# Kernel optimization log

Measured on AMD Instinct MI355X. Metric: run time of the kernel, lower is better.

The kernel has to match this reference:

```python
import jax, jax.numpy as jnp
import numpy as np

NEG_SLOPE_MLP = 0.1   # F.leaky_relu(x, 0.1) used throughout the repo
NEG_SLOPE_GAT = 0.2   # PyG GATv2Conv default negative_slope
HEADS = 2
OUT = 8


def lrelu(x):
    return jax.nn.leaky_relu(x, NEG_SLOPE_MLP)


def gatv2_conv(x, src, dst, e_attr, wl, bl, wr, br, we, att, bias):
    """PyG-style GATv2Conv with edge features, concat heads.
    x: [N, Din], src/dst: [E], e_attr: [E, 2]
    wl/wr: [heads*out, Din], we: [heads*out, 2], att: [heads, out], bias: [heads*out]
    """
    N = x.shape[0]
    xl = (x @ wl.T + bl).reshape(N, HEADS, OUT)   # source transform
    xr = (x @ wr.T + br).reshape(N, HEADS, OUT)   # target transform
    e = (e_attr @ we.T).reshape(-1, HEADS, OUT)
    m = jax.nn.leaky_relu(xl[src] + xr[dst] + e, NEG_SLOPE_GAT)   # [E, H, O]
    logits = jnp.einsum('ehd,hd->eh', m, att)                      # [E, H]
    # numerically-stable segment softmax over incoming edges of each dst node
    mx = jax.ops.segment_max(logits, dst, num_segments=N)          # [N, H]
    a = jnp.exp(logits - mx[dst])
    denom = jax.ops.segment_sum(a, dst, num_segments=N)
    alpha = a / (denom[dst] + 1e-16)                               # [E, H]
    out = jax.ops.segment_sum(xl[src] * alpha[..., None], dst, num_segments=N)
    return out.reshape(N, HEADS * OUT) + bias                      # [N, 16]


def setup_inputs() -> dict:
    key = jax.random.key(0)
    ks = iter(jax.random.split(key, 64))
    N, E = 250000, 5000000
    inp = {
        'x': jax.random.normal(next(ks), (N, 3), jnp.float32),
        'edge_index': jax.random.randint(next(ks), (2, E), 0, N, jnp.int32),
        'edge_attr': jax.random.normal(next(ks), (E, 2), jnp.float32),
        'meta_data': jax.random.normal(next(ks), (6,), jnp.float32),
    }
    shapes = dict(
        ft1_w=(8, 3), ft1_b=(8,), ft2_w=(8, 8), ft2_b=(8,),
        g1_wl=(16, 8), g1_bl=(16,), g1_wr=(16, 8), g1_br=(16,), g1_we=(16, 2), g1_att=(2, 8), g1_bias=(16,),
        g2_wl=(16, 16), g2_bl=(16,), g2_wr=(16, 16), g2_br=(16,), g2_we=(16, 2), g2_att=(2, 8), g2_bias=(16,),
        sp1_w=(64, 16), sp1_b=(64,), sp2_w=(16, 64), sp2_b=(16,),
        me_w=(8, 6), me_b=(8,),
        fc1_w=(24, 24), fc1_b=(24,), fc2_w=(8, 24), fc2_b=(8,), fc3_w=(3, 8), fc3_b=(3,),
    )
    for name, shp in shapes.items():
        inp[name] = 0.2 * jax.random.normal(next(ks), shp, jnp.float32)
    return inp


def reference(x, edge_index, edge_attr, meta_data,
              ft1_w, ft1_b, ft2_w, ft2_b,
              g1_wl, g1_bl, g1_wr, g1_br, g1_we, g1_att, g1_bias,
              g2_wl, g2_bl, g2_wr, g2_br, g2_we, g2_att, g2_bias,
              sp1_w, sp1_b, sp2_w, sp2_b, me_w, me_b,
              fc1_w, fc1_b, fc2_w, fc2_b, fc3_w, fc3_b):
    src, dst = edge_index[0], edge_index[1]
    # tiny per-node MLP feature transform
    h = lrelu(x @ ft1_w.T + ft1_b)
    h = lrelu(h @ ft2_w.T + ft2_b)                              # [N, 8]
    # 2-layer GATv2 block (activation between layers)
    h = gatv2_conv(h, src, dst, edge_attr, g1_wl, g1_bl, g1_wr, g1_br, g1_we, g1_att, g1_bias)
    h = lrelu(h)
    h = gatv2_conv(h, src, dst, edge_attr, g2_wl, g2_bl, g2_wr, g2_br, g2_we, g2_att, g2_bias)  # [N, 16]
    # sum pool over all nodes + small MLP
    p = h.sum(axis=0)                                           # [16]
    p = lrelu(p @ sp1_w.T + sp1_b)
    p = p @ sp2_w.T + sp2_b                                     # [16]
    # meta data encoder
    m = lrelu(meta_data @ me_w.T + me_b)                        # [8]
    z = jnp.concatenate([p, m], axis=0)                         # [24]
    z = lrelu(z @ fc1_w.T + fc1_b)
    z = lrelu(z @ fc2_w.T + fc2_b)
    # dropout is identity in eval/reference mode
    z = z @ fc3_w.T + fc3_b                                     # [3]
    return jax.nn.softmax(z[None, :], axis=1)                   # [1, 3]
```

## Files before the change

kernel.cpp:

```cpp
#include <hip/hip_runtime.h>
#include <hip/hip_bf16.h>
#include <hip/hip_fp16.h>
#include <math.h>


#define HO 16
#define BSHIFT 8
#define BNODES 256
#define PT 512
#define PCHUNK 6144
#define CAP2 6016
#define CAPB 1984

typedef __attribute__((ext_vector_type(2))) float v2f;
typedef __attribute__((ext_vector_type(4))) float v4f;

__device__ __forceinline__ float lrelu(float x, float s) { return x > 0.f ? x : s * x; }

__device__ __forceinline__ uint2 pack_fp8x8(const float* v) {
    int a = __builtin_amdgcn_cvt_pk_fp8_f32(v[0], v[1], 0, false);
    a     = __builtin_amdgcn_cvt_pk_fp8_f32(v[2], v[3], a, true);
    int b = __builtin_amdgcn_cvt_pk_fp8_f32(v[4], v[5], 0, false);
    b     = __builtin_amdgcn_cvt_pk_fp8_f32(v[6], v[7], b, true);
    return make_uint2((unsigned int)a, (unsigned int)b);
}

__device__ __forceinline__ void unpack_fp8x8(uint2 u, float* v) {
    v2f f0 = __builtin_amdgcn_cvt_pk_f32_fp8((int)u.x, false);
    v2f f1 = __builtin_amdgcn_cvt_pk_f32_fp8((int)u.x, true);
    v2f f2 = __builtin_amdgcn_cvt_pk_f32_fp8((int)u.y, false);
    v2f f3 = __builtin_amdgcn_cvt_pk_f32_fp8((int)u.y, true);
    v[0]=f0.x; v[1]=f0.y; v[2]=f1.x; v[3]=f1.y;
    v[4]=f2.x; v[5]=f2.y; v[6]=f3.x; v[7]=f3.y;
}

__global__ void __launch_bounds__(256) node_l1(
    const float* __restrict__ x,
    const float* __restrict__ ft1_w, const float* __restrict__ ft1_b,
    const float* __restrict__ ft2_w, const float* __restrict__ ft2_b,
    const float* __restrict__ wl, const float* __restrict__ bl,
    const float* __restrict__ wr, const float* __restrict__ br,
    uint2* __restrict__ xlA, float* __restrict__ xr, int N)
{
    int n = blockIdx.x * 256 + threadIdx.x;
    if (n >= N) return;
    float x0 = x[3*n], x1 = x[3*n+1], x2 = x[3*n+2];
    float h1[8];
#pragma unroll
    for (int j = 0; j < 8; j++) {
        float a = ft1_w[3*j]*x0 + ft1_w[3*j+1]*x1 + ft1_w[3*j+2]*x2 + ft1_b[j];
        h1[j] = lrelu(a, 0.1f);
    }
    float h2[8];
#pragma unroll
    for (int j = 0; j < 8; j++) {
        float a = ft2_b[j];
#pragma unroll
        for (int k = 0; k < 8; k++) a += ft2_w[8*j+k]*h1[k];
        h2[j] = lrelu(a, 0.1f);
    }
    float ol[HO], orr[HO];
#pragma unroll
    for (int j = 0; j < HO; j++) {
        float a = bl[j], b = br[j];
#pragma unroll
        for (int k = 0; k < 8; k++) { a += wl[8*j+k]*h2[k]; b += wr[8*j+k]*h2[k]; }
        ol[j] = a; orr[j] = b;
    }
    uint2 p0 = pack_fp8x8(ol);
    uint2 p1 = pack_fp8x8(ol + 8);
    ((uint4*)xlA)[n] = make_uint4(p0.x, p0.y, p1.x, p1.y);
    float4* xr4 = (float4*)(xr + (size_t)n*HO);
#pragma unroll
    for (int q = 0; q < 4; q++)
        xr4[q] = make_float4(orr[4*q], orr[4*q+1], orr[4*q+2], orr[4*q+3]);
}

__global__ void __launch_bounds__(256) k_binit(int* __restrict__ bcur)
{
    int b = blockIdx.x * 256 + threadIdx.x;
    if (b < 1024) bcur[b] = b * CAP2;
}

__global__ void __launch_bounds__(PT) k_part(
    const int* __restrict__ src, const int* __restrict__ dst,
    const float* __restrict__ eattr, int* __restrict__ bcur,
    uint2* __restrict__ grecs, int E)
{
    __shared__ int hist[1024], lofs[1024], gofs[1024], lcur[1024];
    __shared__ int scan_s[PT];
    __shared__ uint2 srecs[PCHUNK];
    __shared__ unsigned short bid[PCHUNK];
    int t = threadIdx.x;
    int base = blockIdx.x * PCHUNK;
    int cnt = E - base; if (cnt > PCHUNK) cnt = PCHUNK;

    for (int b = t; b < 1024; b += PT) hist[b] = 0;
    __syncthreads();
    for (int i = t; i < cnt; i += PT)
        atomicAdd(&hist[dst[base + i] >> BSHIFT], 1);
    __syncthreads();
    int h0 = hist[2*t], h1 = hist[2*t+1];
    int pair = h0 + h1;
    scan_s[t] = pair;
    __syncthreads();
    for (int off = 1; off < PT; off <<= 1) {
        int add = (t >= off) ? scan_s[t - off] : 0;
        __syncthreads();
        scan_s[t] += add;
        __syncthreads();
    }
    int pbase = scan_s[t] - pair;
    lofs[2*t]   = pbase;
    lofs[2*t+1] = pbase + h0;
    __syncthreads();
    for (int b = t; b < 1024; b += PT) {
        int c = hist[b];
        int g = (c > 0) ? atomicAdd(&bcur[b], c) : 0;
        gofs[b] = g - lofs[b];
        lcur[b] = 0;
    }
    __syncthreads();
    for (int i = t; i < cnt; i += PT) {
        int e = base + i;
        int d = dst[e];
        int b = d >> BSHIFT;
        float2 ea = ((const float2*)eattr)[e];
        __half2 hv = __floats2half2_rn(ea.x, ea.y);
        unsigned int eb = *reinterpret_cast<unsigned int*>(&hv);
        int q = atomicAdd(&lcur[b], 1);
        int idx = lofs[b] + q;
        srecs[idx] = make_uint2(((unsigned int)src[e] << 8) | (unsigned int)(d & (BNODES-1)), eb);
        bid[idx] = (unsigned short)b;
    }
    __syncthreads();
    for (int i = t; i < cnt; i += PT) {
        int b = bid[i];
        int pos = gofs[b] + i;
        if (pos < (b + 1) * CAP2) grecs[pos] = srecs[i];
    }
}

__global__ void __launch_bounds__(256) k_fine(
    const int* __restrict__ bcur, uint2* recs,
    int* __restrict__ rowS, int* __restrict__ rowE, int N)
{
    __shared__ uint2 rout[CAP2];
    __shared__ int lhist[256], lsc[256], lcur2[256];
    int b = blockIdx.x;
    int bstart = b * CAP2;
    int cnt = bcur[b] - bstart;
    if (cnt > CAP2) cnt = CAP2;
    if (cnt < 0) cnt = 0;
    int t = threadIdx.x;
    lhist[t] = 0;
    __syncthreads();
    for (int i = t; i < cnt; i += 256)
        atomicAdd(&lhist[recs[bstart + i].x & (BNODES-1)], 1);
    __syncthreads();
    int v = lhist[t];
    lsc[t] = v;
    __syncthreads();
    for (int off = 1; off < 256; off <<= 1) {
        int add = (t >= off) ? lsc[t - off] : 0;
        __syncthreads();
        lsc[t] += add;
        __syncthreads();
    }
    int ex = lsc[t] - v;
    lcur2[t] = ex;
    int n = (b << BSHIFT) + t;
    if (n < N) { rowS[n] = bstart + ex; rowE[n] = bstart + ex + v; }
    __syncthreads();
    for (int i = t; i < cnt; i += 256) {
        uint2 r = recs[bstart + i];
        int p = atomicAdd(&lcur2[r.x & (BNODES-1)], 1);
        rout[p] = make_uint2(r.x >> 8, r.y);
    }
    __syncthreads();
    for (int i = t; i < cnt; i += 256)
        recs[bstart + i] = rout[i];
}

struct AggState { float m, s, acc[8]; };

__device__ __forceinline__ void agg_edge(
    AggState& st, const float* va, const float* xd,
    const float* w0, const float* w1, const float* at,
    float ea0, float ea1)
{
    float lg = 0.f;
#pragma unroll
    for (int o = 0; o < 8; o++) {
        float mv = va[o] + xd[o] + (w0[o]*ea0 + w1[o]*ea1);
        mv = mv > 0.f ? mv : 0.2f*mv;
        lg += mv * at[o];
    }
    float nm = fmaxf(st.m, lg);
    float sc = __expf(st.m - nm);
    float wv = __expf(lg - nm);
    st.s = st.s*sc + wv;
#pragma unroll
    for (int o = 0; o < 8; o++) st.acc[o] = st.acc[o]*sc + wv*va[o];
    st.m = nm;
}

__device__ __forceinline__ void agg_lds(
    int t, int nblk0, int N,
    const int* __restrict__ rowS, const int* __restrict__ rowE,
    const uint2* __restrict__ recs, const uint4* __restrict__ xl16,
    uint4* va_s, unsigned int* ea_s,
    bool alive, int rs, int re, int h,
    const float* xd, const float* w0, const float* w1, const float* at,
    AggState& st)
{
    int nlast = nblk0 + 127; if (nlast > N - 1) nlast = N - 1;
    int ebeg = rowS[nblk0];
    int eend = rowE[nlast];
    for (int cbase = ebeg; cbase < eend; cbase += CAPB) {
        int ccnt = eend - cbase; if (ccnt > CAPB) ccnt = CAPB;
        __syncthreads();
        for (int j = t; j < ccnt; j += 256) {
            uint2 r = recs[cbase + j];
            va_s[j] = xl16[r.x];
            ea_s[j] = r.y;
        }
        __syncthreads();
        if (alive) {
            int ls = rs > cbase ? rs : cbase;
            int ce = cbase + ccnt;
            int le = re < ce ? re : ce;
            for (int i = ls; i < le; i++) {
                int j = i - cbase;
                const uint2* vp = reinterpret_cast<const uint2*>(va_s + j);
                uint2 g = vp[h];
                float v[8]; unpack_fp8x8(g, v);
                unsigned int eb = ea_s[j];
                __half2 h2 = *reinterpret_cast<__half2*>(&eb);
                agg_edge(st, v, xd, w0, w1, at, __low2float(h2), __high2float(h2));
            }
        }
    }
}

__global__ void __launch_bounds__(256) node_agg_l1(
    const int* __restrict__ rowS, const int* __restrict__ rowE,
    const uint2* __restrict__ recs,
    const uint4* __restrict__ xlA, float* xr,
    const float* __restrict__ we, const float* __restrict__ att,
    const float* __restrict__ bias,
    const float* __restrict__ wl2, const float* __restrict__ bl2,
    const float* __restrict__ wr2, const float* __restrict__ br2,
    uint2* __restrict__ xlB, int N)
{
    __shared__ uint4 va_s[CAPB];
    __shared__ unsigned int ea_s[CAPB];
    int t = threadIdx.x;
    int tid = blockIdx.x * 256 + t;
    int n = tid >> 1, h = tid & 1;
    bool alive = (n < N);
    int kb = h*8;
    int rs = alive ? rowS[n] : 0;
    int re = alive ? rowE[n] : 0;
    float xd[8], w0[8], w1[8], at[8];
    {
        size_t nn = alive ? (size_t)n : 0;
        const float4* xrp = (const float4*)(xr + nn*HO + kb);
        float4 d0 = xrp[0], d1 = xrp[1];
        xd[0]=d0.x; xd[1]=d0.y; xd[2]=d0.z; xd[3]=d0.w;
        xd[4]=d1.x; xd[5]=d1.y; xd[6]=d1.z; xd[7]=d1.w;
    }
#pragma unroll
    for (int o = 0; o < 8; o++) {
        w0[o] = we[2*(kb+o)];
        w1[o] = we[2*(kb+o)+1];
        at[o] = att[kb+o];
    }
    AggState st;
    st.m = -INFINITY; st.s = 0.f;
#pragma unroll
    for (int o = 0; o < 8; o++) st.acc[o] = 0.f;

    agg_lds(t, blockIdx.x*128, N, rowS, rowE, recs, xlA, va_s, ea_s,
            alive, rs, re, h, xd, w0, w1, at, st);
    if (!alive) return;

    float inv = 1.f/(st.s + 1e-16f);
    float hh[8];
#pragma unroll
    for (int o = 0; o < 8; o++) hh[o] = lrelu(st.acc[o]*inv + bias[kb+o], 0.1f);
    float hfull[HO];
#pragma unroll
    for (int o = 0; o < 8; o++) {
        float hp = __shfl_xor(hh[o], 1, 64);
        hfull[kb + o] = hh[o];
        hfull[(kb ^ 8) + o] = hp;
    }
    float ol[8], orr[8];
#pragma unroll
    for (int jo = 0; jo < 8; jo++) {
        int j = kb + jo;
        float a = bl2[j], b = br2[j];
#pragma unroll
        for (int k = 0; k < HO; k++) { a += wl2[HO*j+k]*hfull[k]; b += wr2[HO*j+k]*hfull[k]; }
        ol[jo] = a; orr[jo] = b;
    }
    xlB[(size_t)n*2 + h] = pack_fp8x8(ol);
    float4* xr4 = (float4*)(xr + (size_t)n*HO + kb);
    xr4[0] = make_float4(orr[0], orr[1], orr[2], orr[3]);
    xr4[1] = make_float4(orr[4], orr[5], orr[6], orr[7]);
}

__global__ void __launch_bounds__(256) node_agg_l2(
    const int* __restrict__ rowS, const int* __restrict__ rowE,
    const uint2* __restrict__ recs,
    const uint4* __restrict__ xlB, const float* __restrict__ xr,
    const float* __restrict__ we, const float* __restrict__ att,
    const float* __restrict__ bias, float* __restrict__ partials, int pstride, int N)
{
    __shared__ uint4 va_s[CAPB];
    __shared__ unsigned int ea_s[CAPB];
    int t = threadIdx.x;
    int tid = blockIdx.x * 256 + t;
    int n = tid >> 1, h = tid & 1;
    bool alive = (n < N);
    int kb = h*8;
    int rs = alive ? rowS[n] : 0;
    int re = alive ? rowE[n] : 0;
    float xd[8], w0[8], w1[8], at[8];
    {
        size_t nn = alive ? (size_t)n : 0;
        const float4* xrp = (const float4*)(xr + nn*HO + kb);
        float4 d0 = xrp[0], d1 = xrp[1];
        xd[0]=d0.x; xd[1]=d0.y; xd[2]=d0.z; xd[3]=d0.w;
        xd[4]=d1.x; xd[5]=d1.y; xd[6]=d1.z; xd[7]=d1.w;
    }
#pragma unroll
    for (int o = 0; o < 8; o++) {
        w0[o] = we[2*(kb+o)];
        w1[o] = we[2*(kb+o)+1];
        at[o] = att[kb+o];
    }
    AggState st;
    st.m = -INFINITY; st.s = 0.f;
#pragma unroll
    for (int o = 0; o < 8; o++) st.acc[o] = 0.f;

    agg_lds(t, blockIdx.x*128, N, rowS, rowE, recs, xlB, va_s, ea_s,
            alive, rs, re, h, xd, w0, w1, at, st);

    float out[8];
    if (alive) {
        float inv = 1.f/(st.s + 1e-16f);
#pragma unroll
        for (int o = 0; o < 8; o++) out[o] = st.acc[o]*inv + bias[kb+o];
    } else {
#pragma unroll
        for (int o = 0; o < 8; o++) out[o] = 0.f;
    }
#pragma unroll
    for (int off = 32; off >= 2; off >>= 1) {
#pragma unroll
        for (int o = 0; o < 8; o++) out[o] += __shfl_down(out[o], off, 64);
    }
    __shared__ float sm[4][2][8];
    int wave = threadIdx.x >> 6, lane = threadIdx.x & 63;
    if (lane < 2) {
#pragma unroll
        for (int o = 0; o < 8; o++) sm[wave][lane][o] = out[o];
    }
    __syncthreads();
    if (threadIdx.x < 16) {
        int hh = threadIdx.x >> 3, oo = threadIdx.x & 7;
        float tt = sm[0][hh][oo] + sm[1][hh][oo] + sm[2][hh][oo] + sm[3][hh][oo];
        partials[(size_t)(hh*8 + oo) * pstride + blockIdx.x] = tt;
    }
}

__global__ void __launch_bounds__(256) k_reduce(
    const float* __restrict__ partials, int pstride, int nparts,
    float* __restrict__ pool)
{
    __shared__ float s[256];
    int c = blockIdx.x;
    int t = threadIdx.x;
    const float* col = partials + (size_t)c * pstride;
    float acc = 0.f;
    for (int r = t; r < nparts; r += 256) acc += col[r];
    s[t] = acc;
    __syncthreads();
#pragma unroll
    for (int off = 128; off > 0; off >>= 1) {
        if (t < off) s[t] += s[t + off];
        __syncthreads();
    }
    if (t == 0) pool[c] = s[0];
}

__global__ void __launch_bounds__(64) final_mlp(
    const float* __restrict__ pool, const float* __restrict__ meta,
    const float* __restrict__ sp1_w, const float* __restrict__ sp1_b,
    const float* __restrict__ sp2_w, const float* __restrict__ sp2_b,
    const float* __restrict__ me_w, const float* __restrict__ me_b,
    const float* __restrict__ fc1_w, const float* __restrict__ fc1_b,
    const float* __restrict__ fc2_w, const float* __restrict__ fc2_b,
    const float* __restrict__ fc3_w, const float* __restrict__ fc3_b,
    float* __restrict__ out)
{
    __shared__ float s1[64], zb[24], z1[24], z2[8];
    int t = threadIdx.x;
    {
        float acc = sp1_b[t];
        for (int k = 0; k < 16; k++) acc += pool[k]*sp1_w[t*16+k];
        s1[t] = lrelu(acc, 0.1f);
    }
    __syncthreads();
    if (t < 16) {
        float acc = sp2_b[t];
        for (int k = 0; k < 64; k++) acc += s1[k]*sp2_w[t*64+k];
        zb[t] = acc;
    } else if (t < 24) {
        int j = t - 16;
        float acc = me_b[j];
        for (int k = 0; k < 6; k++) acc += meta[k]*me_w[j*6+k];
        zb[t] = lrelu(acc, 0.1f);
    }
    __syncthreads();
    if (t < 24) {
        float acc = fc1_b[t];
        for (int k = 0; k < 24; k++) acc += zb[k]*fc1_w[t*24+k];
        z1[t] = lrelu(acc, 0.1f);
    }
    __syncthreads();
    if (t < 8) {
        float acc = fc2_b[t];
        for (int k = 0; k < 24; k++) acc += z1[k]*fc2_w[t*24+k];
        z2[t] = lrelu(acc, 0.1f);
    }
    __syncthreads();
    if (t == 0) {
        float z3[3]; float mxv = -1e30f;
        for (int j = 0; j < 3; j++) {
            float acc = fc3_b[j];
            for (int k = 0; k < 8; k++) acc += z2[k]*fc3_w[j*8+k];
            z3[j] = acc; mxv = fmaxf(mxv, acc);
        }
        float s = 0.f;
        for (int j = 0; j < 3; j++) { z3[j] = __expf(z3[j]-mxv); s += z3[j]; }
        for (int j = 0; j < 3; j++) out[j] = z3[j]/s;
    }
}

extern "C" void kernel_launch(void* const* d_in, const int* in_sizes, int n_in,
                              void* d_out, int out_size, void* d_ws, size_t ws_size,
                              hipStream_t stream)
{
    const float* x      = (const float*)d_in[0];
    const int*   eidx   = (const int*)  d_in[1];
    const float* eattr  = (const float*)d_in[2];
    const float* meta   = (const float*)d_in[3];
    const float* ft1_w  = (const float*)d_in[4];
    const float* ft1_b  = (const float*)d_in[5];
    const float* ft2_w  = (const float*)d_in[6];
    const float* ft2_b  = (const float*)d_in[7];
    const float* g1_wl  = (const float*)d_in[8];
    const float* g1_bl  = (const float*)d_in[9];
    const float* g1_wr  = (const float*)d_in[10];
    const float* g1_br  = (const float*)d_in[11];
    const float* g1_we  = (const float*)d_in[12];
    const float* g1_att = (const float*)d_in[13];
    const float* g1_bias= (const float*)d_in[14];
    const float* g2_wl  = (const float*)d_in[15];
    const float* g2_bl  = (const float*)d_in[16];
    const float* g2_wr  = (const float*)d_in[17];
    const float* g2_br  = (const float*)d_in[18];
    const float* g2_we  = (const float*)d_in[19];
    const float* g2_att = (const float*)d_in[20];
    const float* g2_bias= (const float*)d_in[21];
    const float* sp1_w  = (const float*)d_in[22];
    const float* sp1_b  = (const float*)d_in[23];
    const float* sp2_w  = (const float*)d_in[24];
    const float* sp2_b  = (const float*)d_in[25];
    const float* me_w   = (const float*)d_in[26];
    const float* me_b   = (const float*)d_in[27];
    const float* fc1_w  = (const float*)d_in[28];
    const float* fc1_b  = (const float*)d_in[29];
    const float* fc2_w  = (const float*)d_in[30];
    const float* fc2_b  = (const float*)d_in[31];
    const float* fc3_w  = (const float*)d_in[32];
    const float* fc3_b  = (const float*)d_in[33];
    float* out = (float*)d_out;

    const int N = in_sizes[0] / 3;
    const int E = in_sizes[2] / 2;
    const int* src = eidx;
    const int* dst = eidx + E;

    const int BN    = (N + 255) / 256;
    const int BN2   = (2*N + 255) / 256;
    const int NBUCK = (N + BNODES - 1) >> BSHIFT;
    const int BP    = (E + PCHUNK - 1) / PCHUNK;
    const int pstride = (BN2 + 63) & ~63;

    char* w = (char*)d_ws;
    size_t off = 0;
    auto take = [&](size_t bytes) { size_t o = off; off += (bytes + 255) & ~(size_t)255; return o; };
    int*    rowS     = (int*)   (w + take((size_t)4*N));
    int*    rowE     = (int*)   (w + take((size_t)4*N));
    int*    bcur     = (int*)   (w + take(4096));
    float*  pool     = (float*) (w + take(64));
    float*  partials = (float*) (w + take((size_t)4*16*pstride));
    uint2*  recs     = (uint2*) (w + take((size_t)8*NBUCK*CAP2));
    uint2*  xlA      = (uint2*) (w + take((size_t)16*N));
    uint2*  xlB      = (uint2*) (w + take((size_t)16*N));
    float*  xr       = (float*) (w + take((size_t)64*N));

    node_l1<<<BN, 256, 0, stream>>>(x, ft1_w, ft1_b, ft2_w, ft2_b,
                                    g1_wl, g1_bl, g1_wr, g1_br, xlA, xr, N);
    k_binit<<<4, 256, 0, stream>>>(bcur);
    k_part<<<BP, PT, 0, stream>>>(src, dst, eattr, bcur, recs, E);
    k_fine<<<NBUCK, 256, 0, stream>>>(bcur, recs, rowS, rowE, N);

    node_agg_l1<<<BN2, 256, 0, stream>>>(rowS, rowE, recs, (const uint4*)xlA, xr,
                                         g1_we, g1_att, g1_bias,
                                         g2_wl, g2_bl, g2_wr, g2_br, xlB, N);
    node_agg_l2<<<BN2, 256, 0, stream>>>(rowS, rowE, recs, (const uint4*)xlB, xr,
                                         g2_we, g2_att, g2_bias, partials, pstride, N);
    k_reduce<<<16, 256, 0, stream>>>(partials, pstride, BN2, pool);
    final_mlp<<<1, 64, 0, stream>>>(pool, meta, sp1_w, sp1_b, sp2_w, sp2_b,
                                    me_w, me_b, fc1_w, fc1_b, fc2_w, fc2_b,
                                    fc3_w, fc3_b, out);
}
```

Measured before the change: 442.3 us.

## Replace LDS-staged edge gather with direct per-thread gathers and head-split warps

The aggregation kernels no longer stage each block's edge records and source features into shared memory behind block-wide barriers. Each thread now walks its own CSR row and gathers the 8-byte fp8 half-feature for its head straight from global memory, with a 4-way unrolled loop to keep several loads in flight. Threads are remapped so each wave handles a single head for 128 consecutive nodes, which makes the head index wave-uniform. Layer-1 partner exchange moves from a lane shuffle to shared memory, and the launch bounds request higher occupancy. The cost is uncoalesced gathers from global memory, and per-thread loops over rows of different degree can leave lanes of a wave idle.

```diff
diff --git a/kernel.cpp b/kernel.cpp
--- a/kernel.cpp
+++ b/kernel.cpp
@@ -10,10 +10,8 @@
 #define PT 512
 #define PCHUNK 6144
 #define CAP2 6016
-#define CAPB 1984
 
 typedef __attribute__((ext_vector_type(2))) float v2f;
-typedef __attribute__((ext_vector_type(4))) float v4f;
 
 __device__ __forceinline__ float lrelu(float x, float s) { return x > 0.f ? x : s * x; }
 
@@ -205,64 +203,68 @@
     st.m = nm;
 }
 
-__device__ __forceinline__ void agg_lds(
-    int t, int nblk0, int N,
-    const int* __restrict__ rowS, const int* __restrict__ rowE,
-    const uint2* __restrict__ recs, const uint4* __restrict__ xl16,
-    uint4* va_s, unsigned int* ea_s,
-    bool alive, int rs, int re, int h,
+__device__ __forceinline__ void agg_one(
+    AggState& st, uint2 r, uint2 g, const float* xd,
+    const float* w0, const float* w1, const float* at)
+{
+    float v[8];
+    unpack_fp8x8(g, v);
+    __half2 h2 = *reinterpret_cast<__half2*>(&r.y);
+    agg_edge(st, v, xd, w0, w1, at, __low2float(h2), __high2float(h2));
+}
+
+__device__ __forceinline__ void agg_row(
+    int rs, int re, int hu,
+    const uint2* __restrict__ recs, const uint2* __restrict__ xl8,
     const float* xd, const float* w0, const float* w1, const float* at,
     AggState& st)
 {
-    int nlast = nblk0 + 127; if (nlast > N - 1) nlast = N - 1;
-    int ebeg = rowS[nblk0];
-    int eend = rowE[nlast];
-    for (int cbase = ebeg; cbase < eend; cbase += CAPB) {
-        int ccnt = eend - cbase; if (ccnt > CAPB) ccnt = CAPB;
-        __syncthreads();
-        for (int j = t; j < ccnt; j += 256) {
-            uint2 r = recs[cbase + j];
-            va_s[j] = xl16[r.x];
-            ea_s[j] = r.y;
-        }
-        __syncthreads();
-        if (alive) {
-            int ls = rs > cbase ? rs : cbase;
-            int ce = cbase + ccnt;
-            int le = re < ce ? re : ce;
-            for (int i = ls; i < le; i++) {
-                int j = i - cbase;
-                const uint2* vp = reinterpret_cast<const uint2*>(va_s + j);
-                uint2 g = vp[h];
-                float v[8]; unpack_fp8x8(g, v);
-                unsigned int eb = ea_s[j];
-                __half2 h2 = *reinterpret_cast<__half2*>(&eb);
-                agg_edge(st, v, xd, w0, w1, at, __low2float(h2), __high2float(h2));
-            }
-        }
-    }
-}
-
-__global__ void __launch_bounds__(256) node_agg_l1(
+    st.m = -INFINITY; st.s = 0.f;
+#pragma unroll
+    for (int o = 0; o < 8; o++) st.acc[o] = 0.f;
+    int i = rs;
+    for (; i + 4 <= re; i += 4) {
+        uint2 r0 = recs[i], r1 = recs[i+1], r2 = recs[i+2], r3 = recs[i+3];
+        uint2 g0 = xl8[(size_t)r0.x*2 + hu];
+        uint2 g1 = xl8[(size_t)r1.x*2 + hu];
+        uint2 g2 = xl8[(size_t)r2.x*2 + hu];
+        uint2 g3 = xl8[(size_t)r3.x*2 + hu];
+        agg_one(st, r0, g0, xd, w0, w1, at);
+        agg_one(st, r1, g1, xd, w0, w1, at);
+        agg_one(st, r2, g2, xd, w0, w1, at);
+        agg_one(st, r3, g3, xd, w0, w1, at);
+    }
+    for (; i < re; i++) {
+        uint2 r0 = recs[i];
+        uint2 g0 = xl8[(size_t)r0.x*2 + hu];
+        agg_one(st, r0, g0, xd, w0, w1, at);
+    }
+}
+
+__global__ void __launch_bounds__(256, 8) node_agg_l1(
     const int* __restrict__ rowS, const int* __restrict__ rowE,
     const uint2* __restrict__ recs,
-    const uint4* __restrict__ xlA, float* xr,
+    const uint2* __restrict__ xlA, float* xr,
     const float* __restrict__ we, const float* __restrict__ att,
     const float* __restrict__ bias,
     const float* __restrict__ wl2, const float* __restrict__ bl2,
     const float* __restrict__ wr2, const float* __restrict__ br2,
     uint2* __restrict__ xlB, int N)
 {
-    __shared__ uint4 va_s[CAPB];
-    __shared__ unsigned int ea_s[CAPB];
+    __shared__ float sh[256][8];
     int t = threadIdx.x;
-    int tid = blockIdx.x * 256 + t;
-    int n = tid >> 1, h = tid & 1;
+    int hu = __builtin_amdgcn_readfirstlane(t >> 7);
+    int n = blockIdx.x * 128 + (t & 127);
     bool alive = (n < N);
-    int kb = h*8;
-    int rs = alive ? rowS[n] : 0;
-    int re = alive ? rowE[n] : 0;
-    float xd[8], w0[8], w1[8], at[8];
+    int kb = hu * 8;
+    float w0[8], w1[8], at[8];
+#pragma unroll
+    for (int o = 0; o < 8; o++) {
+        w0[o] = we[2*(kb+o)];
+        w1[o] = we[2*(kb+o)+1];
+        at[o] = att[kb+o];
+    }
+    float xd[8];
     {
         size_t nn = alive ? (size_t)n : 0;
         const float4* xrp = (const float4*)(xr + nn*HO + kb);
@@ -270,64 +272,64 @@
         xd[0]=d0.x; xd[1]=d0.y; xd[2]=d0.z; xd[3]=d0.w;
         xd[4]=d1.x; xd[5]=d1.y; xd[6]=d1.z; xd[7]=d1.w;
     }
+    int rs = alive ? rowS[n] : 0;
+    int re = alive ? rowE[n] : 0;
+    AggState st;
+    agg_row(rs, re, hu, recs, xlA, xd, w0, w1, at, st);
+
+    float inv = 1.f/(st.s + 1e-16f);
+    float hh[8];
+#pragma unroll
+    for (int o = 0; o < 8; o++) hh[o] = lrelu(st.acc[o]*inv + bias[kb+o], 0.1f);
+#pragma unroll
+    for (int o = 0; o < 8; o++) sh[t][o] = hh[o];
+    __syncthreads();
+    if (!alive) return;
+    int partner = t ^ 128;
+    float h0v[8], h1v[8];
+#pragma unroll
+    for (int o = 0; o < 8; o++) {
+        float oth = sh[partner][o];
+        h0v[o] = hu ? oth : hh[o];
+        h1v[o] = hu ? hh[o] : oth;
+    }
+    float ol[8], orr[8];
+#pragma unroll
+    for (int jo = 0; jo < 8; jo++) {
+        int j = kb + jo;
+        float a = bl2[j], b = br2[j];
+#pragma unroll
+        for (int k = 0; k < 8; k++) { a += wl2[HO*j+k]*h0v[k];   b += wr2[HO*j+k]*h0v[k]; }
+#pragma unroll
+        for (int k = 0; k < 8; k++) { a += wl2[HO*j+8+k]*h1v[k]; b += wr2[HO*j+8+k]*h1v[k]; }
+        ol[jo] = a; orr[jo] = b;
+    }
+    xlB[(size_t)n*2 + hu] = pack_fp8x8(ol);
+    float4* xr4 = (float4*)(xr + (size_t)n*HO + kb);
+    xr4[0] = make_float4(orr[0], orr[1], orr[2], orr[3]);
+    xr4[1] = make_float4(orr[4], orr[5], orr[6], orr[7]);
+}
+
+__global__ void __launch_bounds__(256, 8) node_agg_l2(
+    const int* __restrict__ rowS, const int* __restrict__ rowE,
+    const uint2* __restrict__ recs,
+    const uint2* __restrict__ xlB, const float* __restrict__ xr,
+    const float* __restrict__ we, const float* __restrict__ att,
+    const float* __restrict__ bias, float* __restrict__ partials, int pstride, int N)
+{
+    int t = threadIdx.x;
+    int hu = __builtin_amdgcn_readfirstlane(t >> 7);
+    int n = blockIdx.x * 128 + (t & 127);
+    bool alive = (n < N);
+    int kb = hu * 8;
+    float w0[8], w1[8], at[8];
 #pragma unroll
     for (int o = 0; o < 8; o++) {
         w0[o] = we[2*(kb+o)];
         w1[o] = we[2*(kb+o)+1];
         at[o] = att[kb+o];
     }
-    AggState st;
-    st.m = -INFINITY; st.s = 0.f;
-#pragma unroll
-    for (int o = 0; o < 8; o++) st.acc[o] = 0.f;
-
-    agg_lds(t, blockIdx.x*128, N, rowS, rowE, recs, xlA, va_s, ea_s,
-            alive, rs, re, h, xd, w0, w1, at, st);
-    if (!alive) return;
-
-    float inv = 1.f/(st.s + 1e-16f);
-    float hh[8];
-#pragma unroll
-    for (int o = 0; o < 8; o++) hh[o] = lrelu(st.acc[o]*inv + bias[kb+o], 0.1f);
-    float hfull[HO];
-#pragma unroll
-    for (int o = 0; o < 8; o++) {
-        float hp = __shfl_xor(hh[o], 1, 64);
-        hfull[kb + o] = hh[o];
-        hfull[(kb ^ 8) + o] = hp;
-    }
-    float ol[8], orr[8];
-#pragma unroll
-    for (int jo = 0; jo < 8; jo++) {
-        int j = kb + jo;
-        float a = bl2[j], b = br2[j];
-#pragma unroll
-        for (int k = 0; k < HO; k++) { a += wl2[HO*j+k]*hfull[k]; b += wr2[HO*j+k]*hfull[k]; }
-        ol[jo] = a; orr[jo] = b;
-    }
-    xlB[(size_t)n*2 + h] = pack_fp8x8(ol);
-    float4* xr4 = (float4*)(xr + (size_t)n*HO + kb);
-    xr4[0] = make_float4(orr[0], orr[1], orr[2], orr[3]);
-    xr4[1] = make_float4(orr[4], orr[5], orr[6], orr[7]);
-}
-
-__global__ void __launch_bounds__(256) node_agg_l2(
-    const int* __restrict__ rowS, const int* __restrict__ rowE,
-    const uint2* __restrict__ recs,
-    const uint4* __restrict__ xlB, const float* __restrict__ xr,
-    const float* __restrict__ we, const float* __restrict__ att,
-    const float* __restrict__ bias, float* __restrict__ partials, int pstride, int N)
-{
-    __shared__ uint4 va_s[CAPB];
-    __shared__ unsigned int ea_s[CAPB];
-    int t = threadIdx.x;
-    int tid = blockIdx.x * 256 + t;
-    int n = tid >> 1, h = tid & 1;
-    bool alive = (n < N);
-    int kb = h*8;
-    int rs = alive ? rowS[n] : 0;
-    int re = alive ? rowE[n] : 0;
-    float xd[8], w0[8], w1[8], at[8];
+    float xd[8];
     {
         size_t nn = alive ? (size_t)n : 0;
         const float4* xrp = (const float4*)(xr + nn*HO + kb);
@@ -335,19 +337,10 @@
         xd[0]=d0.x; xd[1]=d0.y; xd[2]=d0.z; xd[3]=d0.w;
         xd[4]=d1.x; xd[5]=d1.y; xd[6]=d1.z; xd[7]=d1.w;
     }
-#pragma unroll
-    for (int o = 0; o < 8; o++) {
-        w0[o] = we[2*(kb+o)];
-        w1[o] = we[2*(kb+o)+1];
-        at[o] = att[kb+o];
-    }
+    int rs = alive ? rowS[n] : 0;
+    int re = alive ? rowE[n] : 0;
     AggState st;
-    st.m = -INFINITY; st.s = 0.f;
-#pragma unroll
-    for (int o = 0; o < 8; o++) st.acc[o] = 0.f;
-
-    agg_lds(t, blockIdx.x*128, N, rowS, rowE, recs, xlB, va_s, ea_s,
-            alive, rs, re, h, xd, w0, w1, at, st);
+    agg_row(rs, re, hu, recs, xlB, xd, w0, w1, at, st);
 
     float out[8];
     if (alive) {
@@ -359,21 +352,21 @@
         for (int o = 0; o < 8; o++) out[o] = 0.f;
     }
 #pragma unroll
-    for (int off = 32; off >= 2; off >>= 1) {
+    for (int off = 32; off >= 1; off >>= 1) {
 #pragma unroll
         for (int o = 0; o < 8; o++) out[o] += __shfl_down(out[o], off, 64);
     }
-    __shared__ float sm[4][2][8];
-    int wave = threadIdx.x >> 6, lane = threadIdx.x & 63;
-    if (lane < 2) {
-#pragma unroll
-        for (int o = 0; o < 8; o++) sm[wave][lane][o] = out[o];
-    }
-    __syncthreads();
-    if (threadIdx.x < 16) {
-        int hh = threadIdx.x >> 3, oo = threadIdx.x & 7;
-        float tt = sm[0][hh][oo] + sm[1][hh][oo] + sm[2][hh][oo] + sm[3][hh][oo];
-        partials[(size_t)(hh*8 + oo) * pstride + blockIdx.x] = tt;
+    __shared__ float sm[4][8];
+    int wave = t >> 6, lane = t & 63;
+    if (lane == 0) {
+#pragma unroll
+        for (int o = 0; o < 8; o++) sm[wave][o] = out[o];
+    }
+    __syncthreads();
+    if (t < 16) {
+        int hp = t >> 3, oo = t & 7;
+        float tt = sm[2*hp][oo] + sm[2*hp+1][oo];
+        partials[(size_t)(hp*8 + oo) * pstride + blockIdx.x] = tt;
     }
 }
 
@@ -521,10 +514,10 @@
     k_part<<<BP, PT, 0, stream>>>(src, dst, eattr, bcur, recs, E);
     k_fine<<<NBUCK, 256, 0, stream>>>(bcur, recs, rowS, rowE, N);
 
-    node_agg_l1<<<BN2, 256, 0, stream>>>(rowS, rowE, recs, (const uint4*)xlA, xr,
+    node_agg_l1<<<BN2, 256, 0, stream>>>(rowS, rowE, recs, xlA, xr,
                                          g1_we, g1_att, g1_bias,
                                          g2_wl, g2_bl, g2_wr, g2_br, xlB, N);
-    node_agg_l2<<<BN2, 256, 0, stream>>>(rowS, rowE, recs, (const uint4*)xlB, xr,
+    node_agg_l2<<<BN2, 256, 0, stream>>>(rowS, rowE, recs, xlB, xr,
                                          g2_we, g2_att, g2_bias, partials, pstride, N);
     k_reduce<<<16, 256, 0, stream>>>(partials, pstride, BN2, pool);
     final_mlp<<<1, 64, 0, stream>>>(pool, meta, sp1_w, sp1_b, sp2_w, sp2_b,
```

Result: slower. 465.8 us (+5.3%).
